# Kernel tuning notes

Measured on AMD Instinct MI355X. Metric: run time of the kernel, lower is better.

## Reference

```python
import jax, jax.numpy as jnp
import numpy as np
from jax import lax

W_BCE, W_DICE, W_FT, W_HD = 1.0, 1.0, 1.0, 0.1
TV_ALPHA, TV_BETA, TV_GAMMA = 0.7, 0.3, 0.75
HD_MAX_DIST, HD_BK = 10, 3
SMOOTH, EPS, HD_EPS = 1e-6, 1e-7, 1e-8


def _max_pool(x, k):
    # torch F.max_pool2d pads with -inf implicitly
    pad = k // 2
    return lax.reduce_window(x, -jnp.inf, lax.max, (1, 1, k, k), (1, 1, 1, 1),
                             [(0, 0), (0, 0), (pad, pad), (pad, pad)])


def _min_pool(x, k):
    pad = k // 2
    return lax.reduce_window(x, jnp.inf, lax.min, (1, 1, k, k), (1, 1, 1, 1),
                             [(0, 0), (0, 0), (pad, pad), (pad, pad)])


def _soft_boundary(mask, k):
    dil = _max_pool(mask, k)
    ero = _min_pool(mask, k)  # == -max_pool(-mask)
    return jnp.maximum(dil - ero, 0.0)


def _bce_with_logits(logits, target):
    # numerically stable: max(x,0) - x*t + log1p(exp(-|x|))
    return jnp.mean(jnp.maximum(logits, 0.0) - logits * target +
                    jnp.log1p(jnp.exp(-jnp.abs(logits))))


def _dice_loss(probs, target):
    p = probs.reshape(probs.shape[0], -1)
    t = target.reshape(target.shape[0], -1)
    inter = jnp.sum(p * t, axis=1)
    denom = jnp.sum(p, axis=1) + jnp.sum(t, axis=1)
    dice = (2.0 * inter + SMOOTH) / (denom + SMOOTH + EPS)
    return jnp.mean(1.0 - dice)


def _focal_tversky(probs, target):
    p = probs.reshape(probs.shape[0], -1)
    t = target.reshape(target.shape[0], -1)
    TP = jnp.sum(p * t, axis=1)
    FP = jnp.sum(p * (1.0 - t), axis=1)
    FN = jnp.sum((1.0 - p) * t, axis=1)
    tv = (TP + SMOOTH) / (TP + TV_ALPHA * FP + TV_BETA * FN + SMOOTH + EPS)
    return jnp.mean(jnp.power(1.0 - tv, TV_GAMMA))


def _hausdorff_surrogate(probs, target):
    pred_b = _soft_boundary(probs, HD_BK)
    gt_b = _soft_boundary(target, HD_BK)
    total = jnp.zeros((), probs.dtype)
    weight_sum = 0.0
    for d in range(1, HD_MAX_DIST + 1):
        pred_d = _max_pool(pred_b, 2 * d + 1)
        gt_d = _max_pool(gt_b, 2 * d + 1)
        w = float(d) / float(HD_MAX_DIST)
        total = total + w * (jnp.mean(jnp.abs(pred_d - gt_b)) +
                             jnp.mean(jnp.abs(gt_d - pred_b)))
        weight_sum += w
    return total / (weight_sum + HD_EPS)


def setup_inputs() -> dict:
    key = jax.random.key(0)
    k1, k2 = jax.random.split(key)
    B, C, H, W = 16, 1, 512, 512
    logits = jax.random.normal(k1, (B, C, H, W), dtype=jnp.float32)
    target = jax.random.randint(k2, (B, C, H, W), 0, 2, dtype=jnp.int32)
    return {"logits": logits, "target": target}


def reference(logits, target):
    t = target.astype(jnp.float32)
    bce = _bce_with_logits(logits, t)
    probs = jax.nn.sigmoid(logits)
    d = _dice_loss(probs, t)
    ft = _focal_tversky(probs, t)
    hd = _hausdorff_surrogate(probs, t)
    return W_BCE * bce + W_DICE * d + W_FT * ft + W_HD * hd
```

## Files before the change

kernel.cpp:

```cpp
#include <hip/hip_runtime.h>
#include <math.h>

namespace {

constexpr int B = 16, H = 512, W = 512;
constexpr int HWc = H * W;
constexpr size_t Nc = (size_t)B * HWc;

constexpr int NSTRIP = 13;
constexpr int CENT = 42;
constexpr int NBAND = 16;
constexpr int NWORK = NSTRIP * NBAND * B * 2;
constexpr int NBCE = B * 64;

template <int CTRL>
__device__ __forceinline__ float dpp_shift1(float v) {
  int i = __float_as_int(v);
  int r = __builtin_amdgcn_update_dpp(i, i, CTRL, 0xF, 0xF, false);
  return __int_as_float(r);
}
__device__ __forceinline__ float hmax3(float v) {
  return fmaxf(fmaxf(dpp_shift1<0x138>(v), v), dpp_shift1<0x130>(v));
}
__device__ __forceinline__ float hmin3(float v) {
  return fminf(fminf(dpp_shift1<0x138>(v), v), dpp_shift1<0x130>(v));
}

__device__ __forceinline__ float wave_sum(float v) {
#pragma unroll
  for (int off = 32; off > 0; off >>= 1) v += __shfl_down(v, off);
  return v;
}

__device__ __forceinline__ float block_reduce_256(float v, float* sm, int tid) {
#pragma unroll
  for (int off = 32; off > 0; off >>= 1) v += __shfl_down(v, off);
  int lane = tid & 63, wid = tid >> 6;
  if (lane == 0) sm[wid] = v;
  __syncthreads();
  float r = 0.f;
  if (tid == 0) r = sm[0] + sm[1] + sm[2] + sm[3];
  __syncthreads();
  return r;
}

__global__ void __launch_bounds__(256) bce_kernel(
    const float* __restrict__ logits, const int* __restrict__ target,
    float* __restrict__ bceA, float* __restrict__ spA, float* __restrict__ stA,
    float* __restrict__ sptA) {
  __shared__ float smr[4];
  int img = blockIdx.x >> 6, seg = blockIdx.x & 63;
  const float4* L4 =
      (const float4*)(logits + (size_t)img * HWc + (size_t)seg * 4096);
  const int4* T4 =
      (const int4*)(target + (size_t)img * HWc + (size_t)seg * 4096);
  int tid = threadIdx.x;
  float s_bce = 0.f, s_p = 0.f, s_t = 0.f, s_pt = 0.f;
#pragma unroll
  for (int it = 0; it < 4; ++it) {
    float4 x4 = L4[it * 256 + tid];
    int4 t4 = T4[it * 256 + tid];
    float xs[4] = {x4.x, x4.y, x4.z, x4.w};
    int ts[4] = {t4.x, t4.y, t4.z, t4.w};
#pragma unroll
    for (int j = 0; j < 4; ++j) {
      float x = xs[j];
      float tf = (float)ts[j];
      float e = __expf(-x);
      float p = __builtin_amdgcn_rcpf(1.f + e);
      s_p += p;
      s_t += tf;
      s_pt += p * tf;
      s_bce += x * (1.f - tf) + __logf(1.f + e);
    }
  }
  float r;
  r = block_reduce_256(s_bce, smr, tid);
  if (tid == 0) bceA[blockIdx.x] = r;
  r = block_reduce_256(s_p, smr, tid);
  if (tid == 0) spA[blockIdx.x] = r;
  r = block_reduce_256(s_t, smr, tid);
  if (tid == 0) stA[blockIdx.x] = r;
  r = block_reduce_256(s_pt, smr, tid);
  if (tid == 0) sptA[blockIdx.x] = r;
}

template <int CH, bool EDGE>
__device__ __forceinline__ float load_src(const float* __restrict__ Lg,
                                          const int* __restrict__ Tg, int gy,
                                          int colc) {
  if constexpr (EDGE) gy = min(max(gy, 0), H - 1);
  if constexpr (CH == 0) {
    float x = Lg[gy * W + colc];
    float e = __expf(-x);
    return __builtin_amdgcn_rcpf(1.f + e);
  } else {
    return (float)Tg[gy * W + colc];
  }
}

template <int D>
__device__ __forceinline__ void dilate_steps(float (&a)[52],
                                             const float (&o)[32],
                                             float& acc) {
  if constexpr (D <= 10) {
    float hp = hmax3(a[D - 1]);
    float hc = hmax3(a[D]);
#pragma unroll
    for (int r = D; r <= 51 - D; ++r) {
      float hn = hmax3(a[r + 1]);
      float nv = fmaxf(fmaxf(hp, hc), hn);
      hp = hc;
      hc = hn;
      a[r] = nv;
    }
    constexpr float wd = 0.1f * (float)D;
#pragma unroll
    for (int k = 0; k < 32; ++k) acc += wd * fabsf(a[10 + k] - o[k]);
    dilate_steps<D + 1>(a, o, acc);
  }
}

template <int CH, bool EDGE>
__device__ __forceinline__ void fused_body(const float* __restrict__ Lg,
                                           const int* __restrict__ Tg,
                                           int lane, int strip, int band,
                                           int bz,
                                           float* __restrict__ chain_p) {
  int col = strip * CENT - 11 + lane;
  int colc = min(max(col, 0), W - 1);
  int y0 = band * 32;

  float o[32];
  {
    float v0 = load_src<1 - CH, EDGE>(Lg, Tg, y0 - 1, colc);
    float v1 = load_src<1 - CH, EDGE>(Lg, Tg, y0, colc);
    float hx0 = hmax3(v0), hn0 = hmin3(v0);
    float hx1 = hmax3(v1), hn1 = hmin3(v1);
#pragma unroll
    for (int k = 0; k < 32; ++k) {
      float v2 = load_src<1 - CH, EDGE>(Lg, Tg, y0 + 1 + k, colc);
      float hx2 = hmax3(v2), hn2 = hmin3(v2);
      o[k] = fmaxf(fmaxf(hx0, hx1), hx2) - fminf(fminf(hn0, hn1), hn2);
      hx0 = hx1;
      hx1 = hx2;
      hn0 = hn1;
      hn1 = hn2;
    }
  }

  float a[52];
  {
    float v0 = load_src<CH, EDGE>(Lg, Tg, y0 - 11, colc);
    float v1 = load_src<CH, EDGE>(Lg, Tg, y0 - 10, colc);
    float hx0 = hmax3(v0), hn0 = hmin3(v0);
    float hx1 = hmax3(v1), hn1 = hmin3(v1);
#pragma unroll
    for (int r = 0; r < 52; ++r) {
      float v2 = load_src<CH, EDGE>(Lg, Tg, y0 - 9 + r, colc);
      float hx2 = hmax3(v2), hn2 = hmin3(v2);
      a[r] = fmaxf(fmaxf(hx0, hx1), hx2) - fminf(fminf(hn0, hn1), hn2);
      hx0 = hx1;
      hx1 = hx2;
      hn0 = hn1;
      hn1 = hn2;
    }
  }

  float acc = 0.f;
  dilate_steps<1>(a, o, acc);

  bool valid = (lane >= 11 && lane <= 52 && col < W);
  acc = valid ? acc : 0.f;
  acc = wave_sum(acc);
  if (lane == 0) chain_p[(bz * NBAND + band) * NSTRIP + strip] = acc;
}

__global__ void __launch_bounds__(256, 4) fused_kernel(
    const float* __restrict__ logits, const int* __restrict__ target,
    float* __restrict__ chain_p) {
  int tid = threadIdx.x;
  int lane = tid & 63;
  int wv = tid >> 6;
  int widx = blockIdx.x * 4 + wv;
  int strip = widx % NSTRIP;
  int rest = widx / NSTRIP;
  int band = rest & 15;
  int bz = rest >> 4;
  int img = bz & 15, chain = bz >> 4;
  const float* Lg = logits + (size_t)img * HWc;
  const int* Tg = target + (size_t)img * HWc;
  bool edge = (band == 0) | (band == 15);
  if (chain == 0) {
    if (edge)
      fused_body<0, true>(Lg, Tg, lane, strip, band, bz, chain_p);
    else
      fused_body<0, false>(Lg, Tg, lane, strip, band, bz, chain_p);
  } else {
    if (edge)
      fused_body<1, true>(Lg, Tg, lane, strip, band, bz, chain_p);
    else
      fused_body<1, false>(Lg, Tg, lane, strip, band, bz, chain_p);
  }
}

__global__ void finalize_kernel(const float* __restrict__ bceA,
                                const float* __restrict__ spA,
                                const float* __restrict__ stA,
                                const float* __restrict__ sptA,
                                const float* __restrict__ chain_p,
                                float* __restrict__ out) {
  __shared__ float smr[4];
  __shared__ float smImg[16][3];
  __shared__ double smd[16][2];
  int tid = threadIdx.x;

  float s = 0.f;
  for (int i = tid; i < NBCE; i += 256) s += bceA[i];
  float bce_sum = block_reduce_256(s, smr, tid);

  s = 0.f;
  for (int i = tid; i < NWORK; i += 256) s += chain_p[i];
  float hd_sum = block_reduce_256(s, smr, tid);

  {
    int img = tid >> 4, part = tid & 15;
    float sp = 0.f, st = 0.f, spt = 0.f;
    for (int j = part; j < 64; j += 16) {
      int idx = img * 64 + j;
      sp += spA[idx];
      st += stA[idx];
      spt += sptA[idx];
    }
#pragma unroll
    for (int off = 8; off > 0; off >>= 1) {
      sp += __shfl_down(sp, off, 16);
      st += __shfl_down(st, off, 16);
      spt += __shfl_down(spt, off, 16);
    }
    if (part == 0) {
      smImg[img][0] = sp;
      smImg[img][1] = st;
      smImg[img][2] = spt;
    }
  }
  __syncthreads();
  if (tid < 16) {
    double sp = smImg[tid][0], st = smImg[tid][1], spt = smImg[tid][2];
    double dice = (2.0 * spt + 1e-6) / (sp + st + 1e-6 + 1e-7);
    double tv = (spt + 1e-6) /
                (spt + 0.7 * (sp - spt) + 0.3 * (st - spt) + 1e-6 + 1e-7);
    smd[tid][0] = 1.0 - dice;
    smd[tid][1] = pow(1.0 - tv, 0.75);
  }
  __syncthreads();
  if (tid == 0) {
    double dice_l = 0.0, ft_l = 0.0;
    for (int i = 0; i < 16; ++i) {
      dice_l += smd[i][0];
      ft_l += smd[i][1];
    }
    dice_l /= 16.0;
    ft_l /= 16.0;
    const double Nd = (double)Nc;
    double bce = (double)bce_sum / Nd;
    double hd = ((double)hd_sum / Nd) / (5.5 + 1e-8);
    out[0] = (float)(bce + dice_l + ft_l + 0.1 * hd);
  }
}

}

extern "C" void kernel_launch(void* const* d_in, const int* in_sizes, int n_in,
                              void* d_out, int out_size, void* d_ws,
                              size_t ws_size, hipStream_t stream) {
  const float* logits = (const float*)d_in[0];
  const int* target = (const int*)d_in[1];
  float* out = (float*)d_out;

  float* part = (float*)d_ws;
  float* bceA = part;
  float* spA = part + NBCE;
  float* stA = part + 2 * NBCE;
  float* sptA = part + 3 * NBCE;
  float* chain_p = part + 4 * NBCE;

  bce_kernel<<<dim3(NBCE), dim3(256), 0, stream>>>(logits, target, bceA, spA,
                                                   stA, sptA);
  fused_kernel<<<dim3(NWORK / 4), dim3(256), 0, stream>>>(logits, target,
                                                          chain_p);
  finalize_kernel<<<1, 256, 0, stream>>>(bceA, spA, stA, sptA, chain_p, out);
}
```

Measured before the change: 140.4 us.

## Merge BCE reduction kernel into fused kernel and split HD accumulator

Folds the BCE/dice/tversky partial-sum kernel into the fused Hausdorff kernel as extra leading blocks, removing one launch and letting the memory-bound BCE blocks overlap with the compute-heavy dilation blocks. Also splits the per-lane Hausdorff accumulator into four independent partial sums to shorten the dependent add chain. Risks: the merged kernel shares one launch-bounds/register budget, and the BCE blocks dispatched first may delay the long dilation tail.

```diff
diff --git a/kernel.cpp b/kernel.cpp
--- a/kernel.cpp
+++ b/kernel.cpp
@@ -11,6 +11,7 @@
 constexpr int CENT = 42;
 constexpr int NBAND = 16;
 constexpr int NWORK = NSTRIP * NBAND * B * 2;
+constexpr int NSB = NWORK / 4;
 constexpr int NBCE = B * 64;
 
 template <int CTRL>
@@ -19,6 +20,7 @@
   int r = __builtin_amdgcn_update_dpp(i, i, CTRL, 0xF, 0xF, false);
   return __int_as_float(r);
 }
+
 __device__ __forceinline__ float hmax3(float v) {
   return fmaxf(fmaxf(dpp_shift1<0x138>(v), v), dpp_shift1<0x130>(v));
 }
@@ -42,47 +44,6 @@
   if (tid == 0) r = sm[0] + sm[1] + sm[2] + sm[3];
   __syncthreads();
   return r;
-}
-
-__global__ void __launch_bounds__(256) bce_kernel(
-    const float* __restrict__ logits, const int* __restrict__ target,
-    float* __restrict__ bceA, float* __restrict__ spA, float* __restrict__ stA,
-    float* __restrict__ sptA) {
-  __shared__ float smr[4];
-  int img = blockIdx.x >> 6, seg = blockIdx.x & 63;
-  const float4* L4 =
-      (const float4*)(logits + (size_t)img * HWc + (size_t)seg * 4096);
-  const int4* T4 =
-      (const int4*)(target + (size_t)img * HWc + (size_t)seg * 4096);
-  int tid = threadIdx.x;
-  float s_bce = 0.f, s_p = 0.f, s_t = 0.f, s_pt = 0.f;
-#pragma unroll
-  for (int it = 0; it < 4; ++it) {
-    float4 x4 = L4[it * 256 + tid];
-    int4 t4 = T4[it * 256 + tid];
-    float xs[4] = {x4.x, x4.y, x4.z, x4.w};
-    int ts[4] = {t4.x, t4.y, t4.z, t4.w};
-#pragma unroll
-    for (int j = 0; j < 4; ++j) {
-      float x = xs[j];
-      float tf = (float)ts[j];
-      float e = __expf(-x);
-      float p = __builtin_amdgcn_rcpf(1.f + e);
-      s_p += p;
-      s_t += tf;
-      s_pt += p * tf;
-      s_bce += x * (1.f - tf) + __logf(1.f + e);
-    }
-  }
-  float r;
-  r = block_reduce_256(s_bce, smr, tid);
-  if (tid == 0) bceA[blockIdx.x] = r;
-  r = block_reduce_256(s_p, smr, tid);
-  if (tid == 0) spA[blockIdx.x] = r;
-  r = block_reduce_256(s_t, smr, tid);
-  if (tid == 0) stA[blockIdx.x] = r;
-  r = block_reduce_256(s_pt, smr, tid);
-  if (tid == 0) sptA[blockIdx.x] = r;
 }
 
 template <int CH, bool EDGE>
@@ -102,7 +63,7 @@
 template <int D>
 __device__ __forceinline__ void dilate_steps(float (&a)[52],
                                              const float (&o)[32],
-                                             float& acc) {
+                                             float (&accv)[4]) {
   if constexpr (D <= 10) {
     float hp = hmax3(a[D - 1]);
     float hc = hmax3(a[D]);
@@ -116,8 +77,8 @@
     }
     constexpr float wd = 0.1f * (float)D;
 #pragma unroll
-    for (int k = 0; k < 32; ++k) acc += wd * fabsf(a[10 + k] - o[k]);
-    dilate_steps<D + 1>(a, o, acc);
+    for (int k = 0; k < 32; ++k) accv[k & 3] += wd * fabsf(a[10 + k] - o[k]);
+    dilate_steps<D + 1>(a, o, accv);
   }
 }
 
@@ -167,8 +128,9 @@
     }
   }
 
-  float acc = 0.f;
-  dilate_steps<1>(a, o, acc);
+  float accv[4] = {0.f, 0.f, 0.f, 0.f};
+  dilate_steps<1>(a, o, accv);
+  float acc = (accv[0] + accv[1]) + (accv[2] + accv[3]);
 
   bool valid = (lane >= 11 && lane <= 52 && col < W);
   acc = valid ? acc : 0.f;
@@ -176,13 +138,62 @@
   if (lane == 0) chain_p[(bz * NBAND + band) * NSTRIP + strip] = acc;
 }
 
+__device__ __forceinline__ void bce_body(const float* __restrict__ logits,
+                                         const int* __restrict__ target,
+                                         int blk, float* __restrict__ bceA,
+                                         float* __restrict__ spA,
+                                         float* __restrict__ stA,
+                                         float* __restrict__ sptA) {
+  __shared__ float smr[4];
+  int img = blk >> 6, seg = blk & 63;
+  const float4* L4 =
+      (const float4*)(logits + (size_t)img * HWc + (size_t)seg * 4096);
+  const int4* T4 =
+      (const int4*)(target + (size_t)img * HWc + (size_t)seg * 4096);
+  int tid = threadIdx.x;
+  float s_bce = 0.f, s_p = 0.f, s_t = 0.f, s_pt = 0.f;
+#pragma unroll
+  for (int it = 0; it < 4; ++it) {
+    float4 x4 = L4[it * 256 + tid];
+    int4 t4 = T4[it * 256 + tid];
+    float xs[4] = {x4.x, x4.y, x4.z, x4.w};
+    int ts[4] = {t4.x, t4.y, t4.z, t4.w};
+#pragma unroll
+    for (int j = 0; j < 4; ++j) {
+      float x = xs[j];
+      float tf = (float)ts[j];
+      float e = __expf(-x);
+      float p = __builtin_amdgcn_rcpf(1.f + e);
+      s_p += p;
+      s_t += tf;
+      s_pt += p * tf;
+      s_bce += x * (1.f - tf) + __logf(1.f + e);
+    }
+  }
+  float r;
+  r = block_reduce_256(s_bce, smr, tid);
+  if (tid == 0) bceA[blk] = r;
+  r = block_reduce_256(s_p, smr, tid);
+  if (tid == 0) spA[blk] = r;
+  r = block_reduce_256(s_t, smr, tid);
+  if (tid == 0) stA[blk] = r;
+  r = block_reduce_256(s_pt, smr, tid);
+  if (tid == 0) sptA[blk] = r;
+}
+
 __global__ void __launch_bounds__(256, 4) fused_kernel(
     const float* __restrict__ logits, const int* __restrict__ target,
+    float* __restrict__ bceA, float* __restrict__ spA,
+    float* __restrict__ stA, float* __restrict__ sptA,
     float* __restrict__ chain_p) {
+  if (blockIdx.x < NBCE) {
+    bce_body(logits, target, blockIdx.x, bceA, spA, stA, sptA);
+    return;
+  }
   int tid = threadIdx.x;
   int lane = tid & 63;
   int wv = tid >> 6;
-  int widx = blockIdx.x * 4 + wv;
+  int widx = (blockIdx.x - NBCE) * 4 + wv;
   int strip = widx % NSTRIP;
   int rest = widx / NSTRIP;
   int band = rest & 15;
@@ -285,9 +296,7 @@
   float* sptA = part + 3 * NBCE;
   float* chain_p = part + 4 * NBCE;
 
-  bce_kernel<<<dim3(NBCE), dim3(256), 0, stream>>>(logits, target, bceA, spA,
-                                                   stA, sptA);
-  fused_kernel<<<dim3(NWORK / 4), dim3(256), 0, stream>>>(logits, target,
-                                                          chain_p);
+  fused_kernel<<<dim3(NBCE + NSB), dim3(256), 0, stream>>>(
+      logits, target, bceA, spA, stA, sptA, chain_p);
   finalize_kernel<<<1, 256, 0, stream>>>(bceA, spA, stA, sptA, chain_p, out);
 }
```

New measurement: 139.2 us. About the same (-0.9%).
